# Kernel tuning notes

Hardware: AMD Instinct MI355X
Metric: run time of the kernel (lower is better)

Reference implementation:

```python
import jax, jax.numpy as jnp
import numpy as np
import math

B, N, D = 128, 64, 2
H, M, L = 64, 64, 2
OMEGA = 1.0


def setup_inputs() -> dict:
    key = jax.random.key(0)
    ks = jax.random.split(key, 32)
    s = 0.1  # param scale
    rn = lambda k, shp: jax.random.normal(k, shp, dtype=jnp.float32) * s
    inp = {
        "x": jax.random.normal(ks[0], (B, N, D), dtype=jnp.float32),
        "spin": jnp.zeros((B, N, 1), jnp.float32),
        "node_w1": rn(ks[1], (D + 1, H)), "node_b1": rn(ks[2], (H,)),
        "node_w2": rn(ks[3], (H, H)), "node_b2": rn(ks[4], (H,)),
        "edge_w1": rn(ks[5], (D + 2, M)), "edge_b1": rn(ks[6], (M,)),
        "edge_w2": rn(ks[7], (M, M)), "edge_b2": rn(ks[8], (M,)),
        "v2e_w1": rn(ks[9], (L, H + M, M)), "v2e_b1": rn(ks[10], (L, M)),
        "v2e_w2": rn(ks[11], (L, M, M)), "v2e_b2": rn(ks[12], (L, M)),
        "e2v_w1": rn(ks[13], (L, M, H)), "e2v_b1": rn(ks[14], (L, H)),
        "e2v_w2": rn(ks[15], (L, H, H)), "e2v_b2": rn(ks[16], (L, H)),
        "head_w1": rn(ks[17], (H, H)), "head_b1": rn(ks[18], (H,)),
        "head_w2": rn(ks[19], (H, D)), "head_b2": rn(ks[20], (D,)),
        # bf_scale_init=0.3 -> softplus-inverse
        "scale": jnp.array([math.log(math.exp(0.3) - 1.0)], jnp.float32),
    }
    return inp


def _mlp(x, w1, b1, w2, b2, act):
    return act(x @ w1 + b1) @ w2 + b2


def reference(x, spin, node_w1, node_b1, node_w2, node_b2,
              edge_w1, edge_b1, edge_w2, edge_b2,
              v2e_w1, v2e_b1, v2e_w2, v2e_b2,
              e2v_w1, e2v_b1, e2v_w2, e2v_b2,
              head_w1, head_b1, head_w2, head_b2, scale):
    gelu = lambda t: jax.nn.gelu(t, approximate=False)  # torch exact GELU
    b, n, d = x.shape
    xs = x * jnp.float32(math.sqrt(OMEGA))
    # node embedding: [B,N,H]
    hv = _mlp(jnp.concatenate([xs, spin], -1), node_w1, node_b1, node_w2, node_b2, gelu)
    # dense pairwise edge features; dr[b,i,j] = xs[b,j] - xs[b,i]
    dr = xs[:, None, :, :] - xs[:, :, None, :]            # [B,N,N,D]
    r2 = jnp.sum(dr * dr, axis=-1, keepdims=True)          # [B,N,N,1]
    rr = jnp.sqrt(r2 + 1e-12)
    he = _mlp(jnp.concatenate([dr, rr, r2], -1), edge_w1, edge_b1, edge_w2, edge_b2, gelu)  # [B,N,N,M]
    # mask excludes self-edges (i==j) from aggregation (they were never created
    # in the original edge list; their dense entries never influence off-diag values)
    mask = (1.0 - jnp.eye(n, dtype=x.dtype))[None, :, :, None]
    inv = jnp.float32(1.0 / max(n - 1, 1))
    for l in range(v2e_w1.shape[0]):
        hvb = jnp.broadcast_to(hv[:, :, None, :], (b, n, n, hv.shape[-1]))  # source node i
        he = _mlp(jnp.concatenate([hvb, he], -1), v2e_w1[l], v2e_b1[l], v2e_w2[l], v2e_b2[l], gelu)
        m = _mlp(he, e2v_w1[l], e2v_b1[l], e2v_w2[l], e2v_b2[l], gelu)      # [B,N,N,H]
        hv = hv + jnp.sum(m * mask, axis=1) * inv           # scatter-add over sources i into j
    dx = _mlp(hv, head_w1, head_b1, head_w2, head_b2, jnp.tanh) * jax.nn.softplus(scale[0])
    return dx - jnp.mean(dx, axis=1, keepdims=True)
```

## Files before the change

### kernel.cpp

```cpp
#include <hip/hip_runtime.h>
#include <math.h>


typedef unsigned short u16;
typedef unsigned int u32;
typedef _Float16 half8 __attribute__((ext_vector_type(8)));
typedef __attribute__((ext_vector_type(4))) float floatx4;

#define TS 72
#define HROW 72
#define HBLK (64 * HROW)

__device__ __forceinline__ float gelu_f(float x) {
    float s = fabsf(x) * 0.70710678118654752f;
    float q = fmaf(fmaf(fmaf(fmaf(0.078108f, s, 0.000972f), s, 0.230389f), s, 0.278393f), s, 1.0f);
    float q2 = q * q;
    float r = __builtin_amdgcn_rcpf(q2 * q2);
    float t = 0.5f * x * r;
    return x > 0.f ? x - t : t;
}

__global__ __launch_bounds__(256) void k_pre(
    const float* __restrict__ ew2, const float* __restrict__ w1he0,
    const float* __restrict__ w2_0, const float* __restrict__ u1_0,
    const float* __restrict__ w1he1, const float* __restrict__ w2_1,
    const float* __restrict__ u1_1,
    const float* __restrict__ eb2, const float* __restrict__ b2_0,
    const float* __restrict__ c1_0, const float* __restrict__ b2_1,
    const float* __restrict__ c1_1,
    const float* __restrict__ b1_0v, const float* __restrict__ b1nv,
    const float* __restrict__ u2_0, const float* __restrict__ u2_1,
    const float* __restrict__ w1n, const float* __restrict__ hw1,
    _Float16* __restrict__ WF,
    float* __restrict__ biasB, float* __restrict__ biasC, float* __restrict__ biasD,
    float* __restrict__ u2_0T, float* __restrict__ u2_1T,
    float* __restrict__ w1nT, float* __restrict__ hw1T,
    const float* __restrict__ x, const float* __restrict__ spin,
    const float* __restrict__ nw1, const float* __restrict__ nb1,
    const float* __restrict__ nw2, const float* __restrict__ nb2,
    const float* __restrict__ w1_0,
    float* __restrict__ hv, float* __restrict__ p0)
{
    int blk = blockIdx.x;
    if (blk < 64) {
        int s = blk >> 4;
        int idx = (blk & 15) * 256 + threadIdx.x;
        int k = idx >> 6, n = idx & 63;
        const float *A, *Bm;
        if (s == 0)      { A = ew2;  Bm = w1he0; }
        else if (s == 1) { A = w2_0; Bm = u1_0;  }
        else if (s == 2) { A = w2_0; Bm = w1he1; }
        else             { A = w2_1; Bm = u1_1;  }
        float acc = 0.f;
        for (int q = 0; q < 64; ++q) acc = fmaf(A[k * 64 + q], Bm[q * 64 + n], acc);
        int kc = k >> 5, qd = (k >> 3) & 3, jj = k & 7;
        WF[(((s * 2 + kc) * 64 + n) * 4 + qd) * 8 + jj] = (_Float16)acc;
    } else if (blk == 64) {
        int s = threadIdx.x >> 6, cc = threadIdx.x & 63;
        if (s > 0) {
            const float *bv, *Bm, *add; float* dst;
            if (s == 1)      { bv = b2_0; Bm = u1_0;  add = c1_0; dst = biasB; }
            else if (s == 2) { bv = b2_0; Bm = w1he1; add = b1nv; dst = biasC; }
            else             { bv = b2_1; Bm = u1_1;  add = c1_1; dst = biasD; }
            float acc = add[cc];
            for (int q = 0; q < 64; ++q) acc = fmaf(bv[q], Bm[q * 64 + cc], acc);
            dst[cc] = acc;
        }
    } else if (blk < 129) {
        int idx = (blk - 65) * 256 + threadIdx.x;
        int s = idx >> 12, r = idx & 4095, m = r >> 6, tc = r & 63;
        const float* W = s == 0 ? u2_0 : s == 1 ? u2_1 : s == 2 ? w1n : hw1;
        float* WT      = s == 0 ? u2_0T : s == 1 ? u2_1T : s == 2 ? w1nT : hw1T;
        WT[tc * 64 + m] = W[m * 64 + tc];
    } else {
        __shared__ float a[4][64];
        __shared__ float shv[4][64];
        int w = threadIdx.x >> 6, h = threadIdx.x & 63;
        int node = (blk - 129) * 4 + w;
        float2 xv = ((const float2*)x)[node];
        float sp = spin[node];
        float z = fmaf(xv.x, nw1[h], fmaf(xv.y, nw1[64 + h], fmaf(sp, nw1[128 + h], nb1[h])));
        a[w][h] = gelu_f(z);
        float acc = nb2[h];
        for (int k = 0; k < 64; ++k) acc = fmaf(a[w][k], nw2[k * 64 + h], acc);
        hv[node * 64 + h] = acc;
        shv[w][h] = acc;
        float pa = b1_0v[h];
        for (int q = 0; q < 64; ++q) pa = fmaf(eb2[q], w1he0[q * 64 + h], pa);
        for (int k = 0; k < 64; ++k) pa = fmaf(shv[w][k], w1_0[k * 64 + h], pa);
        p0[node * 64 + h] = pa;
    }
}

__device__ __forceinline__ void mfma_acc(
    const _Float16* __restrict__ tA, const _Float16* __restrict__ WF,
    int stage, int c, int quad, int nn, floatx4 acc[4])
{
    int sA = ((nn >> 2) & 3) << 3;
    #pragma unroll
    for (int kc = 0; kc < 2; ++kc) {
        half8 bf = *(const half8*)(WF + (((stage * 2 + kc) * 64 + c) * 4 + quad) * 8);
        int k0 = (kc * 32 + quad * 8) ^ sA;
        #pragma unroll
        for (int mt = 0; mt < 4; ++mt) {
            half8 af = *(const half8*)(tA + (mt * 16 + nn) * TS + k0);
            acc[mt] = __builtin_amdgcn_mfma_f32_16x16x32_f16(af, bf, acc[mt], 0, 0, 0);
        }
    }
}

__device__ __forceinline__ void init_bias(floatx4 acc[4], float bc) {
    #pragma unroll
    for (int mt = 0; mt < 4; ++mt) acc[mt] = (floatx4){bc, bc, bc, bc};
}
__device__ __forceinline__ void init_p(floatx4 acc[4], const float* __restrict__ p,
                                       int rowbase, int c, int quad) {
    #pragma unroll
    for (int mt = 0; mt < 4; ++mt)
        #pragma unroll
        for (int r = 0; r < 4; ++r)
            acc[mt][r] = p[(rowbase + mt * 16 + quad * 4 + r) * 64 + c];
}

__global__ __launch_bounds__(256, 8) void k_L0(
    const float* __restrict__ x,
    const float* __restrict__ ew1, const float* __restrict__ eb1,
    const float* __restrict__ p0,
    const float* __restrict__ biasB,
    const float* __restrict__ u2_0T, const float* __restrict__ c2_0,
    const _Float16* __restrict__ WF,
    const float* __restrict__ hv0, float* __restrict__ hv1,
    const float* __restrict__ w1nT, const float* __restrict__ biasC,
    float* __restrict__ p1,
    u16* __restrict__ he0g)
{
    __shared__ __align__(16) _Float16 tA[64 * TS];
    __shared__ float sS[64];
    __shared__ float shv[64];
    __shared__ float sred[256];
    int t = threadIdx.x, L = t & 63;
    int w = __builtin_amdgcn_readfirstlane(t >> 6);
    int nn = L & 15, quad = L >> 4;
    int c = w * 16 + nn;
    int cw = c ^ (quad << 3);
    int b = blockIdx.x >> 6, j = blockIdx.x & 63;

    float2 xi = ((const float2*)x)[b * 64 + L];
    float2 xj = ((const float2*)x)[b * 64 + j];
    float d0 = xj.x - xi.x, d1 = xj.y - xi.y;
    float r2 = fmaf(d0, d0, d1 * d1);
    float rr = sqrtf(r2 + 1e-12f);
    int swL = ((L >> 2) & 3) << 3;

    #pragma unroll
    for (int mb = 0; mb < 2; ++mb) {
        int m0 = w * 16 + mb * 8;
        half8 h8;
        #pragma unroll
        for (int kk = 0; kk < 8; ++kk) {
            int m = m0 + kk;
            float z = fmaf(d0, ew1[m], fmaf(d1, ew1[64 + m],
                      fmaf(rr, ew1[128 + m], fmaf(r2, ew1[192 + m], eb1[m]))));
            h8[kk] = (_Float16)gelu_f(z);
        }
        *(half8*)(tA + L * TS + (m0 ^ swL)) = h8;
    }
    __syncthreads();

    floatx4 acc[4];
    init_p(acc, p0, b * 64, c, quad);
    mfma_acc(tA, WF, 0, c, quad, nn, acc);
    __syncthreads();
    {
        u16* dst = he0g + (size_t)blockIdx.x * HBLK;
        #pragma unroll
        for (int mt = 0; mt < 4; ++mt)
            #pragma unroll
            for (int r = 0; r < 4; ++r) {
                int i = mt * 16 + quad * 4 + r;
                _Float16 y = (_Float16)gelu_f(acc[mt][r]);
                tA[i * TS + cw] = y;
                dst[i * HROW + cw] = __builtin_bit_cast(u16, y);
            }
    }
    __syncthreads();
    init_bias(acc, biasB[c]);
    mfma_acc(tA, WF, 1, c, quad, nn, acc);
    {
        float s = 0.f;
        #pragma unroll
        for (int mt = 0; mt < 4; ++mt)
            #pragma unroll
            for (int r = 0; r < 4; ++r) {
                int i = mt * 16 + quad * 4 + r;
                float g = gelu_f(acc[mt][r]);
                s += (i == j) ? 0.f : g;
            }
        s += __shfl_xor(s, 16);
        s += __shfl_xor(s, 32);
        if (quad == 0) sS[c] = s;
    }
    __syncthreads();
    {
        const float4* sv4 = (const float4*)(sS + w * 16);
        const float4* uv4 = (const float4*)(u2_0T + L * 64 + w * 16);
        float g = 0.f;
        #pragma unroll
        for (int m4 = 0; m4 < 4; ++m4) {
            float4 sv = sv4[m4], uv = uv4[m4];
            g = fmaf(sv.x, uv.x, fmaf(sv.y, uv.y, fmaf(sv.z, uv.z, fmaf(sv.w, uv.w, g))));
        }
        sred[w * 64 + L] = g;
    }
    __syncthreads();
    if (t < 64) {
        float g = sred[t] + sred[64 + t] + sred[128 + t] + sred[192 + t];
        int o = blockIdx.x * 64 + t;
        float hvv = hv0[o] + g * (1.0f / 63.0f) + c2_0[t];
        hv1[o] = hvv;
        shv[t] = hvv;
    }
    __syncthreads();
    {
        const float4* hv4 = (const float4*)(shv + w * 16);
        const float4* wv4 = (const float4*)(w1nT + L * 64 + w * 16);
        float pa = 0.f;
        #pragma unroll
        for (int m4 = 0; m4 < 4; ++m4) {
            float4 sv = hv4[m4], uv = wv4[m4];
            pa = fmaf(sv.x, uv.x, fmaf(sv.y, uv.y, fmaf(sv.z, uv.z, fmaf(sv.w, uv.w, pa))));
        }
        sred[w * 64 + L] = pa;
    }
    __syncthreads();
    if (t < 64)
        p1[blockIdx.x * 64 + t] = biasC[t] + sred[t] + sred[64 + t] + sred[128 + t] + sred[192 + t];
}

__global__ __launch_bounds__(256, 8) void k_L1(
    const u16* __restrict__ he0g,
    const float* __restrict__ p1,
    const float* __restrict__ biasD,
    const float* __restrict__ u2_1T, const float* __restrict__ c2_1,
    const _Float16* __restrict__ WF,
    const float* __restrict__ hv1,
    const float* __restrict__ hw1T, const float* __restrict__ hb1,
    const float* __restrict__ hw2, const float* __restrict__ hb2,
    const float* __restrict__ scale, float* __restrict__ dx)
{
    __shared__ __align__(16) _Float16 tA[64 * TS];
    __shared__ float sS[64];
    __shared__ float shv[64];
    __shared__ float sred[256];
    int t = threadIdx.x, L = t & 63;
    int w = __builtin_amdgcn_readfirstlane(t >> 6);
    int nn = L & 15, quad = L >> 4;
    int c = w * 16 + nn;
    int cw = c ^ (quad << 3);
    int b = blockIdx.x >> 6, j = blockIdx.x & 63;

    {
        const float4* src = (const float4*)(he0g + (size_t)blockIdx.x * HBLK);
        float4* dstl = (float4*)tA;
        for (int q = t; q < (HBLK * 2 / 16); q += 256)
            dstl[q] = src[q];
    }
    __syncthreads();

    floatx4 acc[4];
    init_p(acc, p1, b * 64, c, quad);
    mfma_acc(tA, WF, 2, c, quad, nn, acc);
    __syncthreads();
    #pragma unroll
    for (int mt = 0; mt < 4; ++mt)
        #pragma unroll
        for (int r = 0; r < 4; ++r)
            tA[(mt * 16 + quad * 4 + r) * TS + cw] = (_Float16)gelu_f(acc[mt][r]);
    __syncthreads();
    init_bias(acc, biasD[c]);
    mfma_acc(tA, WF, 3, c, quad, nn, acc);
    {
        float s = 0.f;
        #pragma unroll
        for (int mt = 0; mt < 4; ++mt)
            #pragma unroll
            for (int r = 0; r < 4; ++r) {
                int i = mt * 16 + quad * 4 + r;
                float g = gelu_f(acc[mt][r]);
                s += (i == j) ? 0.f : g;
            }
        s += __shfl_xor(s, 16);
        s += __shfl_xor(s, 32);
        if (quad == 0) sS[c] = s;
    }
    __syncthreads();
    {
        const float4* sv4 = (const float4*)(sS + w * 16);
        const float4* uv4 = (const float4*)(u2_1T + L * 64 + w * 16);
        float g = 0.f;
        #pragma unroll
        for (int m4 = 0; m4 < 4; ++m4) {
            float4 sv = sv4[m4], uv = uv4[m4];
            g = fmaf(sv.x, uv.x, fmaf(sv.y, uv.y, fmaf(sv.z, uv.z, fmaf(sv.w, uv.w, g))));
        }
        sred[w * 64 + L] = g;
    }
    __syncthreads();
    if (t < 64) {
        float g = sred[t] + sred[64 + t] + sred[128 + t] + sred[192 + t];
        float hv2 = hv1[blockIdx.x * 64 + t] + g * (1.0f / 63.0f) + c2_1[t];
        shv[t] = hv2;
    }
    __syncthreads();
    {
        const float4* hv4 = (const float4*)(shv + w * 16);
        const float4* wv4 = (const float4*)(hw1T + L * 64 + w * 16);
        float a = 0.f;
        #pragma unroll
        for (int m4 = 0; m4 < 4; ++m4) {
            float4 sv = hv4[m4], uv = wv4[m4];
            a = fmaf(sv.x, uv.x, fmaf(sv.y, uv.y, fmaf(sv.z, uv.z, fmaf(sv.w, uv.w, a))));
        }
        sred[w * 64 + L] = a;
    }
    __syncthreads();
    if (t < 64) {
        float a = hb1[t] + sred[t] + sred[64 + t] + sred[128 + t] + sred[192 + t];
        sS[t] = tanhf(a);
    }
    __syncthreads();
    if (t < 64) {
        float t1 = sS[t];
        float dd0 = t1 * hw2[t * 2], dd1 = t1 * hw2[t * 2 + 1];
        #pragma unroll
        for (int off = 1; off <= 32; off <<= 1) { dd0 += __shfl_xor(dd0, off); dd1 += __shfl_xor(dd1, off); }
        if (t == 0) {
            float sp = log1pf(__expf(scale[0]));
            dx[blockIdx.x * 2 + 0] = (dd0 + hb2[0]) * sp;
            dx[blockIdx.x * 2 + 1] = (dd1 + hb2[1]) * sp;
        }
    }
}

__global__ __launch_bounds__(64) void k_mean(
    const float* __restrict__ dx, float* __restrict__ out)
{
    __shared__ float s0[64], s1[64];
    int b = blockIdx.x, j = threadIdx.x;
    float2 d = ((const float2*)dx)[b * 64 + j];
    s0[j] = d.x; s1[j] = d.y;
    __syncthreads();
    float m0 = 0.f, m1 = 0.f;
    for (int q = 0; q < 64; ++q) { m0 += s0[q]; m1 += s1[q]; }
    ((float2*)out)[b * 64 + j] = make_float2(d.x - m0 * (1.0f / 64.0f), d.y - m1 * (1.0f / 64.0f));
}

__global__ void k_beacon(float* out, float code) { out[0] = code; }

extern "C" void kernel_launch(void* const* d_in, const int* in_sizes, int n_in,
                              void* d_out, int out_size, void* d_ws, size_t ws_size,
                              hipStream_t stream)
{
    static const int exp_sizes[23] = {
        16384, 8192, 192, 64, 4096, 64,
        256, 64, 4096, 64,
        16384, 128, 8192, 128,
        8192, 128, 8192, 128,
        4096, 64, 128, 2, 1
    };
    float* hv0 = (float*)d_ws;
    float* hv1 = hv0 + 524288;
    float* p0  = hv1 + 524288;
    float* p1  = p0  + 524288;
    float* dx  = p1  + 524288;
    float* u2_0T = dx + 16384;
    float* u2_1T = u2_0T + 4096;
    float* w1nT  = u2_1T + 4096;
    float* hw1T  = w1nT + 4096;
    float* biasB = hw1T + 4096;
    float* biasC = biasB + 64;
    float* biasD = biasC + 64;
    _Float16* WF = (_Float16*)(biasD + 64);
    u16* he0g  = (u16*)(WF + 16384);
    const size_t need = (size_t)((char*)(he0g + (size_t)8192 * HBLK) - (char*)d_ws);

    int bad = -1;
    if (n_in != 23 || out_size != 16384) bad = 98;
    else if (ws_size < need) bad = 97;
    else for (int i = 0; i < 23; ++i)
        if (in_sizes[i] != exp_sizes[i]) { bad = i; break; }
    if (bad >= 0) {
        k_beacon<<<1, 1, 0, stream>>>((float*)d_out, 2e6f + bad * 1e4f);
        return;
    }

    const float* x      = (const float*)d_in[0];
    const float* spin   = (const float*)d_in[1];
    const float* nw1    = (const float*)d_in[2];
    const float* nb1    = (const float*)d_in[3];
    const float* nw2    = (const float*)d_in[4];
    const float* nb2    = (const float*)d_in[5];
    const float* ew1    = (const float*)d_in[6];
    const float* eb1    = (const float*)d_in[7];
    const float* ew2    = (const float*)d_in[8];
    const float* eb2    = (const float*)d_in[9];
    const float* v2e_w1 = (const float*)d_in[10];
    const float* v2e_b1 = (const float*)d_in[11];
    const float* v2e_w2 = (const float*)d_in[12];
    const float* v2e_b2 = (const float*)d_in[13];
    const float* e2v_w1 = (const float*)d_in[14];
    const float* e2v_b1 = (const float*)d_in[15];
    const float* e2v_w2 = (const float*)d_in[16];
    const float* e2v_b2 = (const float*)d_in[17];
    const float* hw1    = (const float*)d_in[18];
    const float* hb1    = (const float*)d_in[19];
    const float* hw2    = (const float*)d_in[20];
    const float* hb2    = (const float*)d_in[21];
    const float* scale  = (const float*)d_in[22];

    k_pre<<<2177, 256, 0, stream>>>(
        ew2, v2e_w1 + 4096, v2e_w2, e2v_w1,
        v2e_w1 + 12288, v2e_w2 + 4096, e2v_w1 + 4096,
        eb2, v2e_b2, e2v_b1, v2e_b2 + 64, e2v_b1 + 64,
        v2e_b1, v2e_b1 + 64,
        e2v_w2, e2v_w2 + 4096, v2e_w1 + 8192, hw1,
        WF, biasB, biasC, biasD,
        u2_0T, u2_1T, w1nT, hw1T,
        x, spin, nw1, nb1, nw2, nb2, v2e_w1, hv0, p0);
    k_L0<<<8192, 256, 0, stream>>>(x, ew1, eb1,
        p0, biasB, u2_0T, e2v_b2,
        WF, hv0, hv1,
        w1nT, biasC, p1,
        he0g);
    k_L1<<<8192, 256, 0, stream>>>(he0g,
        p1, biasD, u2_1T, e2v_b2 + 64,
        WF, hv1, hw1T, hb1, hw2, hb2, scale, dx);
    k_mean<<<128, 64, 0, stream>>>(dx, (float*)d_out);
}
```

Measured before the change: 226.9 us.

## Fuse mean-centering into k_L1 via last-block atomic and read he0 from global

Removes the separate k_mean launch: each k_L1 block bumps a per-batch atomic counter, and the last block of a batch computes the mean with wave shuffles and writes the centered output. The first MFMA stage of k_L1 now reads the he0 tile straight from global memory instead of staging it in LDS, which drops a copy and a barrier. A redundant syncthreads in the head is also removed. The risks are uncoalesced or repeated global fragment loads in place of LDS reads, plus added atomic and fence cost.

```diff
diff --git a/kernel.cpp b/kernel.cpp
--- a/kernel.cpp
+++ b/kernel.cpp
@@ -35,6 +35,7 @@
     float* __restrict__ biasB, float* __restrict__ biasC, float* __restrict__ biasD,
     float* __restrict__ u2_0T, float* __restrict__ u2_1T,
     float* __restrict__ w1nT, float* __restrict__ hw1T,
+    int* __restrict__ cnt,
     const float* __restrict__ x, const float* __restrict__ spin,
     const float* __restrict__ nw1, const float* __restrict__ nb1,
     const float* __restrict__ nw2, const float* __restrict__ nb2,
@@ -57,7 +58,9 @@
         WF[(((s * 2 + kc) * 64 + n) * 4 + qd) * 8 + jj] = (_Float16)acc;
     } else if (blk == 64) {
         int s = threadIdx.x >> 6, cc = threadIdx.x & 63;
-        if (s > 0) {
+        if (s == 0) {
+            cnt[cc * 2] = 0; cnt[cc * 2 + 1] = 0;
+        } else {
             const float *bv, *Bm, *add; float* dst;
             if (s == 1)      { bv = b2_0; Bm = u1_0;  add = c1_0; dst = biasB; }
             else if (s == 2) { bv = b2_0; Bm = w1he1; add = b1nv; dst = biasC; }
@@ -109,6 +112,23 @@
     }
 }
 
+__device__ __forceinline__ void mfma_acc_g(
+    const u16* __restrict__ gA, const _Float16* __restrict__ WF,
+    int stage, int c, int quad, int nn, floatx4 acc[4])
+{
+    int sA = ((nn >> 2) & 3) << 3;
+    #pragma unroll
+    for (int kc = 0; kc < 2; ++kc) {
+        half8 bf = *(const half8*)(WF + (((stage * 2 + kc) * 64 + c) * 4 + quad) * 8);
+        int k0 = (kc * 32 + quad * 8) ^ sA;
+        #pragma unroll
+        for (int mt = 0; mt < 4; ++mt) {
+            half8 af = *(const half8*)((const _Float16*)gA + (mt * 16 + nn) * HROW + k0);
+            acc[mt] = __builtin_amdgcn_mfma_f32_16x16x32_f16(af, bf, acc[mt], 0, 0, 0);
+        }
+    }
+}
+
 __device__ __forceinline__ void init_bias(floatx4 acc[4], float bc) {
     #pragma unroll
     for (int mt = 0; mt < 4; ++mt) acc[mt] = (floatx4){bc, bc, bc, bc};
@@ -246,12 +266,14 @@
     const float* __restrict__ hv1,
     const float* __restrict__ hw1T, const float* __restrict__ hb1,
     const float* __restrict__ hw2, const float* __restrict__ hb2,
-    const float* __restrict__ scale, float* __restrict__ dx)
+    const float* __restrict__ scale, float* __restrict__ dx,
+    int* __restrict__ cnt, float* __restrict__ out)
 {
     __shared__ __align__(16) _Float16 tA[64 * TS];
     __shared__ float sS[64];
     __shared__ float shv[64];
     __shared__ float sred[256];
+    __shared__ int slast;
     int t = threadIdx.x, L = t & 63;
     int w = __builtin_amdgcn_readfirstlane(t >> 6);
     int nn = L & 15, quad = L >> 4;
@@ -259,18 +281,9 @@
     int cw = c ^ (quad << 3);
     int b = blockIdx.x >> 6, j = blockIdx.x & 63;
 
-    {
-        const float4* src = (const float4*)(he0g + (size_t)blockIdx.x * HBLK);
-        float4* dstl = (float4*)tA;
-        for (int q = t; q < (HBLK * 2 / 16); q += 256)
-            dstl[q] = src[q];
-    }
-    __syncthreads();
-
     floatx4 acc[4];
     init_p(acc, p1, b * 64, c, quad);
-    mfma_acc(tA, WF, 2, c, quad, nn, acc);
-    __syncthreads();
+    mfma_acc_g(he0g + (size_t)blockIdx.x * HBLK, WF, 2, c, quad, nn, acc);
     #pragma unroll
     for (int mt = 0; mt < 4; ++mt)
         #pragma unroll
@@ -326,11 +339,7 @@
     __syncthreads();
     if (t < 64) {
         float a = hb1[t] + sred[t] + sred[64 + t] + sred[128 + t] + sred[192 + t];
-        sS[t] = tanhf(a);
-    }
-    __syncthreads();
-    if (t < 64) {
-        float t1 = sS[t];
+        float t1 = tanhf(a);
         float dd0 = t1 * hw2[t * 2], dd1 = t1 * hw2[t * 2 + 1];
         #pragma unroll
         for (int off = 1; off <= 32; off <<= 1) { dd0 += __shfl_xor(dd0, off); dd1 += __shfl_xor(dd1, off); }
@@ -340,19 +349,22 @@
             dx[blockIdx.x * 2 + 1] = (dd1 + hb2[1]) * sp;
         }
     }
-}
-
-__global__ __launch_bounds__(64) void k_mean(
-    const float* __restrict__ dx, float* __restrict__ out)
-{
-    __shared__ float s0[64], s1[64];
-    int b = blockIdx.x, j = threadIdx.x;
-    float2 d = ((const float2*)dx)[b * 64 + j];
-    s0[j] = d.x; s1[j] = d.y;
-    __syncthreads();
-    float m0 = 0.f, m1 = 0.f;
-    for (int q = 0; q < 64; ++q) { m0 += s0[q]; m1 += s1[q]; }
-    ((float2*)out)[b * 64 + j] = make_float2(d.x - m0 * (1.0f / 64.0f), d.y - m1 * (1.0f / 64.0f));
+    if (t == 0) {
+        __threadfence();
+        slast = (atomicAdd(&cnt[b], 1) == 63);
+    }
+    __syncthreads();
+    if (slast) {
+        __threadfence();
+        if (t < 64) {
+            float2 d = ((const float2*)dx)[b * 64 + t];
+            float m0 = d.x, m1 = d.y;
+            #pragma unroll
+            for (int off = 1; off <= 32; off <<= 1) { m0 += __shfl_xor(m0, off); m1 += __shfl_xor(m1, off); }
+            ((float2*)out)[b * 64 + t] = make_float2(d.x - m0 * (1.0f / 64.0f),
+                                                     d.y - m1 * (1.0f / 64.0f));
+        }
+    }
 }
 
 __global__ void k_beacon(float* out, float code) { out[0] = code; }
@@ -380,7 +392,8 @@
     float* biasB = hw1T + 4096;
     float* biasC = biasB + 64;
     float* biasD = biasC + 64;
-    _Float16* WF = (_Float16*)(biasD + 64);
+    int*   cnt   = (int*)(biasD + 64);
+    _Float16* WF = (_Float16*)(cnt + 128);
     u16* he0g  = (u16*)(WF + 16384);
     const size_t need = (size_t)((char*)(he0g + (size_t)8192 * HBLK) - (char*)d_ws);
 
@@ -425,7 +438,7 @@
         v2e_b1, v2e_b1 + 64,
         e2v_w2, e2v_w2 + 4096, v2e_w1 + 8192, hw1,
         WF, biasB, biasC, biasD,
-        u2_0T, u2_1T, w1nT, hw1T,
+        u2_0T, u2_1T, w1nT, hw1T, cnt,
         x, spin, nw1, nb1, nw2, nb2, v2e_w1, hv0, p0);
     k_L0<<<8192, 256, 0, stream>>>(x, ew1, eb1,
         p0, biasB, u2_0T, e2v_b2,
@@ -434,6 +447,6 @@
         he0g);
     k_L1<<<8192, 256, 0, stream>>>(he0g,
         p1, biasD, u2_1T, e2v_b2 + 64,
-        WF, hv1, hw1T, hb1, hw2, hb2, scale, dx);
-    k_mean<<<128, 64, 0, stream>>>(dx, (float*)d_out);
-}
+        WF, hv1, hw1T, hb1, hw2, hb2, scale, dx,
+        cnt, (float*)d_out);
+}
```

Result: slower. 502.6 us (+121.5%).
